# Optimization experiments

Measured on AMD Instinct MI355X. Metric: run time of the kernel, lower is better.

The kernel has to match this reference:

```python
import jax, jax.numpy as jnp
import numpy as np

B, L, D = 8, 4096, 768
NC = L          # compact slots == max_len (compact_tensors_batch = zeros_like(tensors_batch))
N_CH = L // 2   # actual chunk-id range


def setup_inputs() -> dict:
    key = jax.random.key(0)
    k1, k2, k3, k4, k5 = jax.random.split(key, 5)
    tensors_batch = jax.random.normal(k1, (B, L, D), jnp.float32)
    # sorted segment ids -> contiguous ragged chunks per row; skipped ids are empty slots
    seg_ids = jnp.sort(jax.random.randint(k2, (B, L), 0, N_CH), axis=-1).astype(jnp.int32)
    # chunk-constant masks (the module asserts any()==all() within a chunk)
    pad_len = jax.random.randint(k3, (B, 1), N_CH // 2, N_CH)
    chunk_pad = (jnp.arange(N_CH)[None, :] < pad_len).astype(jnp.int32)          # 1 = real token
    chunk_reg = jax.random.randint(k4, (B, N_CH), 0, 2).astype(jnp.int32)
    chunk_sp = jnp.broadcast_to((jnp.arange(N_CH)[None, :] >= N_CH // 2).astype(jnp.int32), (B, N_CH))
    padding_mask = jnp.take_along_axis(chunk_pad, seg_ids, axis=1)
    regular_tokens_mask = jnp.take_along_axis(chunk_reg, seg_ids, axis=1)
    seq_pair_mask = jnp.take_along_axis(chunk_sp, seg_ids, axis=1)
    # gen_net params: mean-pool over chunk -> Linear(D,D) -> tanh
    W = jax.random.normal(k5, (D, D), jnp.float32) / np.float32(np.sqrt(D))
    b = jnp.zeros((D,), jnp.float32)
    return {"tensors_batch": tensors_batch, "seg_ids": seg_ids,
            "padding_mask": padding_mask, "regular_tokens_mask": regular_tokens_mask,
            "seq_pair_mask": seq_pair_mask, "W": W, "b": b}


def _seg_sum(x, sid):
    return jax.ops.segment_sum(x, sid, num_segments=NC)


def reference(tensors_batch, seg_ids, padding_mask, regular_tokens_mask, seq_pair_mask, W, b):
    f32 = jnp.float32
    counts = jax.vmap(_seg_sum)(jnp.ones((B, L), f32), seg_ids)                  # [B,NC]
    sums = jax.vmap(_seg_sum)(tensors_batch, seg_ids)                            # [B,NC,D]
    mean = sums / jnp.maximum(counts, 1.0)[..., None]
    joint = jnp.tanh(jnp.einsum('bnd,de->bne', mean, W) + b)                     # gen_net
    compact = jnp.where(counts[..., None] > 0, joint, 0.0)                       # scatter into zeros
    pad_any = jax.vmap(_seg_sum)(padding_mask.astype(f32), seg_ids) > 0
    reg_any = jax.vmap(_seg_sum)(regular_tokens_mask.astype(f32), seg_ids) > 0
    sp_sum = jax.vmap(_seg_sum)(seq_pair_mask.astype(f32), seg_ids)
    sp_all = (sp_sum == counts) & (counts > 0)                                   # prod != 0 over chunk
    mask_padding = pad_any.astype(jnp.int32)
    mask_regular = reg_any.astype(jnp.int32)
    mask_seq_pair = jnp.where(mask_padding == 0, -1, sp_all.astype(jnp.int32))
    # column trimming (mask_padding.sum(0)==0) is data-dependent-shape; zero instead of slice
    keep = (mask_padding.sum(axis=0) > 0)                                        # [NC]
    compact_out = compact * keep[None, :, None]
    mask_padding_o = mask_padding * keep[None, :]
    mask_regular_o = mask_regular * keep[None, :]
    mask_seq_pair_o = mask_seq_pair * keep[None, :]
    compression_rate = jnp.sum(mask_regular_o).astype(f32) / jnp.sum(regular_tokens_mask).astype(f32)
    return compact_out, mask_padding_o, mask_regular_o, mask_seq_pair_o, compression_rate
```

## Files before the change

### kernel.cpp

```cpp
#include <hip/hip_runtime.h>
#include <math.h>

#define B_   8
#define L_   4096
#define D_   768
#define NC_  4096
#define NCH_ 2048
#define M_   (B_*NC_)
#define MC_  (B_*NCH_)
#define NKT_ 24
#define META_BLOCKS 128
#define WPREP_BLOCKS 144
#define GEMM_BLOCKS 256
#define MEAN_ZB 512

typedef __attribute__((ext_vector_type(8))) short short8;
typedef __attribute__((ext_vector_type(4))) float f32x4;
typedef unsigned int u32;
typedef unsigned short u16;

__device__ __forceinline__ void gload16(const void* g, void* l) {
    __builtin_amdgcn_global_load_lds((const __attribute__((address_space(1))) u32*)g,
                                     (__attribute__((address_space(3))) u32*)l, 16, 0, 0);
}

__device__ __forceinline__ u16 f2bf(float f) {
    union { float f; u32 u; } v; v.f = f;
    u32 r = v.u + 0x7fffu + ((v.u >> 16) & 1u);
    return (u16)(r >> 16);
}

__device__ __forceinline__ float tanh_fast(float x) {
    float e = __builtin_amdgcn_exp2f(x * 2.885390081777927f);
    return 1.f - 2.f * __builtin_amdgcn_rcpf(e + 1.f);
}

__device__ __forceinline__ size_t aplane_byte(int mc) {
    int span = mc >> 12;
    int rem  = mc & 4095;
    return (size_t)(span * 4096 + 2048) * 3072 + (size_t)rem * 1536;
}

__device__ __forceinline__ int lower_bound(const int* __restrict__ a, int lo, int hi, int v) {
    while (lo < hi) {
        int mid = (lo + hi) >> 1;
        if (a[mid] < v) lo = mid + 1; else hi = mid;
    }
    return lo;
}

__global__ void fused_meta_kernel(const int* __restrict__ seg,
                                  const int* __restrict__ padm,
                                  const int* __restrict__ regm,
                                  const int* __restrict__ spm,
                                  const float* __restrict__ Wm,
                                  u16* __restrict__ wt,
                                  int* __restrict__ counts2, int* __restrict__ starts2,
                                  int* __restrict__ act,
                                  float* __restrict__ out_mp, float* __restrict__ out_mr,
                                  float* __restrict__ out_sp,
                                  float2* __restrict__ partials) {
    __shared__ float shm[64 * 65 + 8];
    int blk = blockIdx.x;
    int t = threadIdx.x;
    if (blk >= META_BLOCKS) {
        int wb = blk - META_BLOCKS;
        int bk = wb % 12, bn = wb / 12;
        int k0 = bk * 64, n0 = bn * 64;
        int ln = t & 63, lw = t >> 6;
        #pragma unroll
        for (int p = 0; p < 16; ++p) {
            int kl = lw + p * 4;
            shm[kl * 65 + ln] = Wm[(size_t)(k0 + kl) * D_ + n0 + ln];
        }
        __syncthreads();
        #pragma unroll
        for (int p = 0; p < 16; ++p) {
            int nl = lw + p * 4;
            wt[(size_t)(n0 + nl) * D_ + k0 + ln] = f2bf(shm[ln * 65 + nl]);
        }
        return;
    }
    int idx = blk * 256 + t;
    int c = idx >> 3, b = idx & 7;
    const int* row = seg + b * L_;
    int s = lower_bound(row, 0, L_, c);
    int e = lower_bound(row, s, L_, c + 1);
    int cnt = e - s;
    counts2[idx] = cnt;
    starts2[idx] = s;
    int mp = 0, mr = 0;
    if (cnt > 0) { mp = padm[b * L_ + s]; mr = regm[b * L_ + s]; }
    int sp = (mp == 0) ? -1 : spm[b * L_ + s];
    int k = mp;
    k |= __shfl_xor(k, 1);
    k |= __shfl_xor(k, 2);
    k |= __shfl_xor(k, 4);
    k = k ? 1 : 0;
    out_mp[b * NC_ + c] = (float)mp;
    out_mr[b * NC_ + c] = (float)(k ? mr : 0);
    out_sp[b * NC_ + c] = (float)(k ? sp : 0);
    if (c < NCH_) act[b * NCH_ + c] = (k && cnt > 0) ? 1 : 0;
    float numP = (float)(k * mr);
    float denP = (float)(cnt * mr);
    #pragma unroll
    for (int off = 32; off; off >>= 1) {
        numP += __shfl_down(numP, off);
        denP += __shfl_down(denP, off);
    }
    __syncthreads();
    if ((t & 63) == 0) { shm[(t >> 6) * 2] = numP; shm[(t >> 6) * 2 + 1] = denP; }
    __syncthreads();
    if (t == 0)
        partials[blk] = make_float2(shm[0] + shm[2] + shm[4] + shm[6],
                                    shm[1] + shm[3] + shm[5] + shm[7]);
}

__global__ void mean_kernel(const float* __restrict__ x,
                            const int* __restrict__ counts2,
                            const int* __restrict__ starts2,
                            char* __restrict__ outb,
                            const float2* __restrict__ partials,
                            float* __restrict__ rateOut) {
    __shared__ float rbuf[4];
    int mc = blockIdx.x;
    int t = threadIdx.x;
    if (mc == MC_ + MEAN_ZB) {
        float n = 0.f, d = 0.f;
        if (t < META_BLOCKS) { float2 p = partials[t]; n = p.x; d = p.y; }
        #pragma unroll
        for (int off = 32; off; off >>= 1) { n += __shfl_down(n, off); d += __shfl_down(d, off); }
        if (t < META_BLOCKS && (t & 63) == 0) { rbuf[(t >> 6) * 2] = n; rbuf[(t >> 6) * 2 + 1] = d; }
        __syncthreads();
        if (t == 0) rateOut[0] = (rbuf[0] + rbuf[2]) / (rbuf[1] + rbuf[3]);
        return;
    }
    if (mc >= MC_) {
        int z = mc - MC_;
        int sp = z >> 7;
        size_t base = (size_t)((4 + sp) * 4096 + 2048) * 3072 + (size_t)(z & 127) * 49152;
        float4* p = (float4*)(outb + base);
        float4 zz = make_float4(0.f, 0.f, 0.f, 0.f);
        #pragma unroll
        for (int i = 0; i < 16; ++i) p[t + i * 192] = zz;
        return;
    }
    int b = mc >> 11, c = mc & (NCH_ - 1);
    int idx = c * 8 + b;
    int cnt = counts2[idx], s = starts2[idx];
    float ax = 0.f, ay = 0.f, az = 0.f, aw = 0.f;
    if (cnt > 0) {
        const float4* base = (const float4*)(x + ((size_t)b * L_ + s) * D_) + t;
        for (int tk = 0; tk < cnt; ++tk) {
            float4 v = base[tk * 192];
            ax += v.x; ay += v.y; az += v.z; aw += v.w;
        }
        float inv = 1.f / (float)cnt;
        ax *= inv; ay *= inv; az *= inv; aw *= inv;
    }
    u16* hi = (u16*)(outb + aplane_byte(mc));
    ushort4 h;
    h.x = f2bf(ax); h.y = f2bf(ay); h.z = f2bf(az); h.w = f2bf(aw);
    *(ushort4*)(hi + 4 * t) = h;
}

__global__ __launch_bounds__(512, 2) void gemm8_kernel(
        const char* __restrict__ aBytes,
        const u16* __restrict__ wt,
        const float* __restrict__ bias,
        const int* __restrict__ act,
        float* __restrict__ out) {
    __shared__ char sA[4 * 8192];
    __shared__ char sB[4 * 24576];
    int bid = blockIdx.x;
    int wg = (bid & 7) * 32 + (bid >> 3);
    int mtile = wg >> 1, ntile = wg & 1;
    int m0 = mtile << 7, n0 = ntile * 384;
    int t = threadIdx.x;
    int lane = t & 63, w = t >> 6;
    int wm = w >> 2, wn = w & 3;

    const char* aT = aBytes + aplane_byte(m0);
    const char* bT = (const char*)(wt + (size_t)n0 * D_);

    int rA = t >> 2, sA_ = t & 3;
    int srcA = rA * 1536 + ((sA_ ^ ((rA ^ (rA >> 2)) & 3)) << 4);
    int srcB[3];
    #pragma unroll
    for (int j = 0; j < 3; ++j) {
        int i = t + j * 512;
        int r = i >> 2, s = i & 3;
        srcB[j] = r * 1536 + ((s ^ ((r ^ (r >> 2)) & 3)) << 4);
    }
    int db = w * 1024;

    int aoff[4], boff[6];
    #pragma unroll
    for (int f = 0; f < 4; ++f) {
        int r = wm * 64 + f * 16 + (lane & 15);
        aoff[f] = r * 64 + ((((lane >> 4)) ^ ((r ^ (r >> 2)) & 3)) << 4);
    }
    #pragma unroll
    for (int g = 0; g < 6; ++g) {
        int r = wn * 96 + g * 16 + (lane & 15);
        boff[g] = r * 64 + ((((lane >> 4)) ^ ((r ^ (r >> 2)) & 3)) << 4);
    }

    f32x4 acc[4][6] = {};

    #pragma unroll
    for (int p = 0; p < 2; ++p) {
        int kof = p << 6;
        gload16(aT + srcA + kof, sA + p * 8192 + db);
        #pragma unroll
        for (int j = 0; j < 3; ++j)
            gload16(bT + srcB[j] + kof, sB + p * 24576 + j * 8192 + db);
    }

    #pragma unroll 1
    for (int kt = 0; kt < NKT_; ++kt) {
        if (kt < NKT_ - 1) asm volatile("s_waitcnt vmcnt(4)" ::: "memory");
        else               asm volatile("s_waitcnt vmcnt(0)" ::: "memory");
        __builtin_amdgcn_s_barrier();
        __builtin_amdgcn_sched_barrier(0);
        const char* curA = sA + (kt & 3) * 8192;
        const char* curB = sB + (kt & 3) * 24576;
        int kn = kt + 2;
        int kof = kn << 6;
        short8 afr[4], bfr[3];
        #pragma unroll
        for (int f = 0; f < 4; ++f) afr[f] = *(const short8*)(curA + aoff[f]);
        #pragma unroll
        for (int g = 0; g < 3; ++g) bfr[g] = *(const short8*)(curB + boff[g]);
        if (kn < NKT_) {
            gload16(aT + srcA + kof, sA + (kn & 3) * 8192 + db);
            gload16(bT + srcB[0] + kof, sB + (kn & 3) * 24576 + db);
        }
        __builtin_amdgcn_s_setprio(1);
        #pragma unroll
        for (int f = 0; f < 4; ++f)
            #pragma unroll
            for (int g = 0; g < 3; ++g)
                acc[f][g] = __builtin_amdgcn_mfma_f32_16x16x32_bf16(
                    afr[f], bfr[g], acc[f][g], 0, 0, 0);
        __builtin_amdgcn_s_setprio(0);
        short8 bfr2[3];
        #pragma unroll
        for (int g = 0; g < 3; ++g) bfr2[g] = *(const short8*)(curB + boff[g + 3]);
        if (kn < NKT_) {
            gload16(bT + srcB[1] + kof, sB + (kn & 3) * 24576 + 8192 + db);
            gload16(bT + srcB[2] + kof, sB + (kn & 3) * 24576 + 16384 + db);
        }
        __builtin_amdgcn_s_setprio(1);
        #pragma unroll
        for (int f = 0; f < 4; ++f)
            #pragma unroll
            for (int g = 0; g < 3; ++g)
                acc[f][g + 3] = __builtin_amdgcn_mfma_f32_16x16x32_bf16(
                    afr[f], bfr2[g], acc[f][g + 3], 0, 0, 0);
        __builtin_amdgcn_s_setprio(0);
        __builtin_amdgcn_sched_barrier(0);
    }

    int ncol[6]; float bs[6];
    #pragma unroll
    for (int g = 0; g < 6; ++g) {
        ncol[g] = n0 + wn * 96 + g * 16 + (lane & 15);
        bs[g] = bias[ncol[g]];
    }
    #pragma unroll
    for (int f = 0; f < 4; ++f) {
        int rbase = m0 + wm * 64 + f * 16 + ((lane >> 4) << 2);
        #pragma unroll
        for (int q = 0; q < 4; ++q) {
            int mc = rbase + q;
            int av = act[mc];
            int gr = mc + ((mc >> 11) << 11);
            size_t orow = (size_t)gr * D_;
            #pragma unroll
            for (int g = 0; g < 6; ++g) {
                float v = av ? tanh_fast(acc[f][g][q] + bs[g]) : 0.f;
                out[orow + ncol[g]] = v;
            }
        }
    }
}

__global__ void zfill0_kernel(char* __restrict__ outb) {
    int z = blockIdx.x;
    int sp = z / 384;
    size_t base = (size_t)(sp * 4096 + 2048) * 3072 + (size_t)(z % 384) * 16384;
    float4* p = (float4*)(outb + base);
    float4 zz = make_float4(0.f, 0.f, 0.f, 0.f);
    int t = threadIdx.x;
    #pragma unroll
    for (int i = 0; i < 4; ++i) p[t + i * 256] = zz;
}

extern "C" void kernel_launch(void* const* d_in, const int* in_sizes, int n_in,
                              void* d_out, int out_size, void* d_ws, size_t ws_size,
                              hipStream_t stream) {
    const float* x    = (const float*)d_in[0];
    const int*   seg  = (const int*)d_in[1];
    const int*   padm = (const int*)d_in[2];
    const int*   regm = (const int*)d_in[3];
    const int*   spm  = (const int*)d_in[4];
    const float* Wm   = (const float*)d_in[5];
    const float* bias = (const float*)d_in[6];
    float* out = (float*)d_out;

    char* ws = (char*)d_ws;
    float2* partials = (float2*)ws;
    int* counts2 = (int*)(ws + 1024);
    int* starts2 = counts2 + M_;
    int* act     = starts2 + M_;
    u16* wt      = (u16*)(act + MC_);

    float* out_mp = out + (size_t)M_ * D_;
    float* out_mr = out_mp + M_;
    float* out_sp = out_mr + M_;
    float* out_rate = out_sp + M_;

    fused_meta_kernel<<<META_BLOCKS + WPREP_BLOCKS, 256, 0, stream>>>(
        seg, padm, regm, spm, Wm, wt, counts2, starts2, act,
        out_mp, out_mr, out_sp, partials);
    mean_kernel<<<MC_ + MEAN_ZB + 1, 192, 0, stream>>>(
        x, counts2, starts2, (char*)d_out, partials, out_rate);
    gemm8_kernel<<<GEMM_BLOCKS, 512, 0, stream>>>(
        (const char*)d_out, wt, bias, act, out);
    zfill0_kernel<<<1536, 256, 0, stream>>>((char*)d_out);
}
```

Baseline: 81.83 us.

## Retile GEMM to 64-row full-width tiles with 3-stage LDS ring and fused zero-fill

The bf16 GEMM now gives each workgroup 64 rows and all 768 output columns, with each of the 8 waves owning 96 columns. Each A tile is therefore read once, at the cost of every block streaming the whole weight matrix. The LDS buffers become a single 156 KB three-stage ring, which drops occupancy to one block per CU. The separate zero-fill kernel is removed; each GEMM block instead zeroes its own staging rows after its main loop, saving a launch but lengthening the GEMM tail.

```diff
diff --git a/kernel.cpp b/kernel.cpp
--- a/kernel.cpp
+++ b/kernel.cpp
@@ -164,45 +164,46 @@
     *(ushort4*)(hi + 4 * t) = h;
 }
 
-__global__ __launch_bounds__(512, 2) void gemm8_kernel(
+__global__ __launch_bounds__(512, 1) void gemm8_kernel(
         const char* __restrict__ aBytes,
         const u16* __restrict__ wt,
         const float* __restrict__ bias,
         const int* __restrict__ act,
         float* __restrict__ out) {
-    __shared__ char sA[4 * 8192];
-    __shared__ char sB[4 * 24576];
+    __shared__ char sAB[159744];
+    char* sA = sAB;
+    char* sB = sAB + 12288;
     int bid = blockIdx.x;
     int wg = (bid & 7) * 32 + (bid >> 3);
-    int mtile = wg >> 1, ntile = wg & 1;
-    int m0 = mtile << 7, n0 = ntile * 384;
+    int m0 = wg << 6;
     int t = threadIdx.x;
     int lane = t & 63, w = t >> 6;
-    int wm = w >> 2, wn = w & 3;
 
     const char* aT = aBytes + aplane_byte(m0);
-    const char* bT = (const char*)(wt + (size_t)n0 * D_);
-
-    int rA = t >> 2, sA_ = t & 3;
-    int srcA = rA * 1536 + ((sA_ ^ ((rA ^ (rA >> 2)) & 3)) << 4);
-    int srcB[3];
-    #pragma unroll
-    for (int j = 0; j < 3; ++j) {
+    const char* bT = (const char*)wt;
+
+    int ta = t & 255;
+    int rA = ta >> 2, sa = ta & 3;
+    int srcA = rA * 1536 + ((sa ^ ((rA ^ (rA >> 2)) & 3)) << 4);
+    int dbA = (w & 3) * 1024;
+    int srcB[6];
+    #pragma unroll
+    for (int j = 0; j < 6; ++j) {
         int i = t + j * 512;
         int r = i >> 2, s = i & 3;
         srcB[j] = r * 1536 + ((s ^ ((r ^ (r >> 2)) & 3)) << 4);
     }
-    int db = w * 1024;
+    int dbB = w * 1024;
 
     int aoff[4], boff[6];
     #pragma unroll
     for (int f = 0; f < 4; ++f) {
-        int r = wm * 64 + f * 16 + (lane & 15);
+        int r = f * 16 + (lane & 15);
         aoff[f] = r * 64 + ((((lane >> 4)) ^ ((r ^ (r >> 2)) & 3)) << 4);
     }
     #pragma unroll
     for (int g = 0; g < 6; ++g) {
-        int r = wn * 96 + g * 16 + (lane & 15);
+        int r = w * 96 + g * 16 + (lane & 15);
         boff[g] = r * 64 + ((((lane >> 4)) ^ ((r ^ (r >> 2)) & 3)) << 4);
     }
 
@@ -211,30 +212,34 @@
     #pragma unroll
     for (int p = 0; p < 2; ++p) {
         int kof = p << 6;
-        gload16(aT + srcA + kof, sA + p * 8192 + db);
-        #pragma unroll
-        for (int j = 0; j < 3; ++j)
-            gload16(bT + srcB[j] + kof, sB + p * 24576 + j * 8192 + db);
-    }
-
+        gload16(aT + srcA + kof, sA + p * 4096 + dbA);
+        #pragma unroll
+        for (int j = 0; j < 6; ++j)
+            gload16(bT + srcB[j] + kof, sB + p * 49152 + j * 8192 + dbB);
+    }
+
+    int cur = 0;
     #pragma unroll 1
     for (int kt = 0; kt < NKT_; ++kt) {
-        if (kt < NKT_ - 1) asm volatile("s_waitcnt vmcnt(4)" ::: "memory");
+        if (kt < NKT_ - 1) asm volatile("s_waitcnt vmcnt(7)" ::: "memory");
         else               asm volatile("s_waitcnt vmcnt(0)" ::: "memory");
         __builtin_amdgcn_s_barrier();
         __builtin_amdgcn_sched_barrier(0);
-        const char* curA = sA + (kt & 3) * 8192;
-        const char* curB = sB + (kt & 3) * 24576;
-        int kn = kt + 2;
-        int kof = kn << 6;
+        const char* curA = sA + cur * 4096;
+        const char* curB = sB + cur * 49152;
+        int nxt = cur + 2; if (nxt >= 3) nxt -= 3;
+        int kof = (kt + 2) << 6;
+        bool st = (kt + 2 < NKT_);
         short8 afr[4], bfr[3];
         #pragma unroll
         for (int f = 0; f < 4; ++f) afr[f] = *(const short8*)(curA + aoff[f]);
         #pragma unroll
         for (int g = 0; g < 3; ++g) bfr[g] = *(const short8*)(curB + boff[g]);
-        if (kn < NKT_) {
-            gload16(aT + srcA + kof, sA + (kn & 3) * 8192 + db);
-            gload16(bT + srcB[0] + kof, sB + (kn & 3) * 24576 + db);
+        if (st) {
+            gload16(aT + srcA + kof, sA + nxt * 4096 + dbA);
+            gload16(bT + srcB[0] + kof, sB + nxt * 49152 + dbB);
+            gload16(bT + srcB[1] + kof, sB + nxt * 49152 + 8192 + dbB);
+            gload16(bT + srcB[2] + kof, sB + nxt * 49152 + 16384 + dbB);
         }
         __builtin_amdgcn_s_setprio(1);
         #pragma unroll
@@ -247,9 +252,10 @@
         short8 bfr2[3];
         #pragma unroll
         for (int g = 0; g < 3; ++g) bfr2[g] = *(const short8*)(curB + boff[g + 3]);
-        if (kn < NKT_) {
-            gload16(bT + srcB[1] + kof, sB + (kn & 3) * 24576 + 8192 + db);
-            gload16(bT + srcB[2] + kof, sB + (kn & 3) * 24576 + 16384 + db);
+        if (st) {
+            gload16(bT + srcB[3] + kof, sB + nxt * 49152 + 24576 + dbB);
+            gload16(bT + srcB[4] + kof, sB + nxt * 49152 + 32768 + dbB);
+            gload16(bT + srcB[5] + kof, sB + nxt * 49152 + 40960 + dbB);
         }
         __builtin_amdgcn_s_setprio(1);
         #pragma unroll
@@ -260,17 +266,18 @@
                     afr[f], bfr2[g], acc[f][g + 3], 0, 0, 0);
         __builtin_amdgcn_s_setprio(0);
         __builtin_amdgcn_sched_barrier(0);
+        if (++cur == 3) cur = 0;
     }
 
     int ncol[6]; float bs[6];
     #pragma unroll
     for (int g = 0; g < 6; ++g) {
-        ncol[g] = n0 + wn * 96 + g * 16 + (lane & 15);
+        ncol[g] = w * 96 + g * 16 + (lane & 15);
         bs[g] = bias[ncol[g]];
     }
     #pragma unroll
     for (int f = 0; f < 4; ++f) {
-        int rbase = m0 + wm * 64 + f * 16 + ((lane >> 4) << 2);
+        int rbase = m0 + f * 16 + ((lane >> 4) << 2);
         #pragma unroll
         for (int q = 0; q < 4; ++q) {
             int mc = rbase + q;
@@ -284,17 +291,11 @@
             }
         }
     }
-}
-
-__global__ void zfill0_kernel(char* __restrict__ outb) {
-    int z = blockIdx.x;
-    int sp = z / 384;
-    size_t base = (size_t)(sp * 4096 + 2048) * 3072 + (size_t)(z % 384) * 16384;
-    float4* p = (float4*)(outb + base);
+
+    float4* pz = (float4*)((char*)out + aplane_byte(m0));
     float4 zz = make_float4(0.f, 0.f, 0.f, 0.f);
-    int t = threadIdx.x;
-    #pragma unroll
-    for (int i = 0; i < 4; ++i) p[t + i * 256] = zz;
+    #pragma unroll
+    for (int i = 0; i < 12; ++i) pz[t + i * 512] = zz;
 }
 
 extern "C" void kernel_launch(void* const* d_in, const int* in_sizes, int n_in,
@@ -328,5 +329,4 @@
         x, counts2, starts2, (char*)d_out, partials, out_rate);
     gemm8_kernel<<<GEMM_BLOCKS, 512, 0, stream>>>(
         (const char*)d_out, wt, bias, act, out);
-    zfill0_kernel<<<1536, 256, 0, stream>>>((char*)d_out);
-}
+}
```

Measured after the change: 71.58 us. 1.14x faster.
